# Kernel optimization log

Hardware: AMD Instinct MI355X
Metric: run time of the kernel (lower is better)

Reference implementation:

```python
import jax, jax.numpy as jnp
import numpy as np

N_NODES = 80000
N_EDGES = 800000
N_REL = 400
D_IN = 256
D_OUT = 256
BN_EPS = 1e-5


def _xavier(key, shape, gain=np.sqrt(2.0)):
    fan_in, fan_out = shape[0], shape[-1]
    std = gain * np.sqrt(2.0 / (fan_in + fan_out))
    return jax.random.normal(key, shape, dtype=jnp.float32) * std


def ccorr(a, b):
    # circular correlation: irfft(conj(rfft(a)) * rfft(b), n)
    n = a.shape[-1]
    return jnp.fft.irfft(jnp.conj(jnp.fft.rfft(a)) * jnp.fft.rfft(b), n)


def setup_inputs() -> dict:
    key = jax.random.key(0)
    ks = jax.random.split(key, 12)
    x = jax.random.normal(ks[0], (N_NODES, D_IN), dtype=jnp.float32)
    rel_repr = jax.random.normal(ks[1], (N_REL, D_IN), dtype=jnp.float32)
    edge_src = jax.random.randint(ks[2], (N_EDGES,), 0, N_NODES)
    edge_dst = jax.random.randint(ks[3], (N_EDGES,), 0, N_NODES)
    edge_type = jax.random.randint(ks[4], (N_EDGES,), 0, N_REL)
    edge_norm = jax.random.uniform(ks[5], (N_EDGES,), dtype=jnp.float32)
    in_w = _xavier(ks[6], (D_IN, D_OUT))
    out_w = _xavier(ks[7], (D_IN, D_OUT))
    loop_w = _xavier(ks[8], (D_IN, D_OUT))
    w_rel = _xavier(ks[9], (D_IN, D_OUT))
    loop_rel = _xavier(ks[10], (1, D_IN))
    bias = jnp.zeros((D_OUT,), dtype=jnp.float32)
    return {"x": x, "rel_repr": rel_repr, "edge_src": edge_src,
            "edge_dst": edge_dst, "edge_type": edge_type, "edge_norm": edge_norm,
            "in_w": in_w, "out_w": out_w, "loop_w": loop_w, "w_rel": w_rel,
            "loop_rel": loop_rel, "bias": bias}


def reference(x, rel_repr, edge_src, edge_dst, edge_type, edge_norm,
              in_w, out_w, loop_w, w_rel, loop_rel, bias):
    E = edge_src.shape[0]
    half = E // 2
    # gather + compose (opn == 'corr')
    h_src = x[edge_src]                         # [E, D_in]
    edge_data = ccorr(h_src, rel_repr[edge_type])  # [E, D_in]
    # direction-split matmul
    msg = jnp.concatenate([edge_data[:half] @ in_w,
                           edge_data[half:] @ out_w], axis=0)  # [E, D_out]
    msg = msg * edge_norm[:, None]
    # scatter-sum into destination nodes, then reduce (dropout p=0, /3)
    agg = jax.ops.segment_sum(msg, edge_dst, num_segments=x.shape[0]) / 3.0
    # self-loop
    loop = ccorr(x, jnp.broadcast_to(loop_rel, x.shape)) @ loop_w / 3.0
    out = agg + loop + bias
    # BatchNorm1d (training mode: batch stats, gamma=1, beta=0)
    mean = jnp.mean(out, axis=0)
    var = jnp.var(out, axis=0)
    out = (out - mean) / jnp.sqrt(var + BN_EPS)
    # act is identity
    return out, rel_repr @ w_rel
```

## Files before the change

### kernel.cpp

```cpp
#include <hip/hip_runtime.h>

#define NN 80000
#define NE 800000
#define EH 400000
#define NR 400
#define DD 256
#define FD 256
#define KP 768
#define NB 160000
#define NCH 157
#define MT 80400
#define PI2 6.283185307179586f

typedef unsigned short u16;
typedef __attribute__((ext_vector_type(8))) short bf16x8;
typedef __attribute__((ext_vector_type(4))) float f32x4;

static __device__ __forceinline__ float bu2f(u16 u) {
  return __uint_as_float(((unsigned int)u) << 16);
}
static __device__ __forceinline__ u16 f2bu(float f) {
  unsigned int x = __float_as_uint(f);
  x += 0x7fffu + ((x >> 16) & 1u);
  return (u16)(x >> 16);
}
static __device__ __forceinline__ unsigned int pk2(float a, float b) {
  return (unsigned int)f2bu(a) | ((unsigned int)f2bu(b) << 16);
}
static __device__ __forceinline__ void gload16(const void* g, void* l) {
  __builtin_amdgcn_global_load_lds(
      (const __attribute__((address_space(1))) unsigned int*)g,
      (__attribute__((address_space(3))) unsigned int*)l, 16, 0, 0);
}

__global__ void k_build_f(u16* __restrict__ Ft) {
  int c = blockIdx.x, j = threadIdx.x;
  int k, im;
  if (c == 0)      { k = 0;   im = 0; }
  else if (c == 1) { k = 128; im = 0; }
  else             { k = c >> 1; im = c & 1; }
  int m = (j * k) & 255;
  float th = -PI2 * (float)m * (1.0f / 256.0f);
  float v = im ? sinf(th) : cosf(th);
  Ft[c * 256 + j] = f2bu(v);
}

__global__ void k_build_m(const float* __restrict__ in_w, const float* __restrict__ out_w,
                          u16* __restrict__ Bt) {
  int t = blockIdx.x;
  int c = threadIdx.x;
  const float* W = (t < 256) ? in_w : out_w;
  int tp = t & 255;
  int k, im; float alpha;
  if (tp == 0)      { k = 0;   im = 0; alpha = 1.0f; }
  else if (tp == 1) { k = 128; im = 0; alpha = 1.0f; }
  else              { k = tp >> 1; im = tp & 1; alpha = 2.0f; }
  float scale = alpha * (1.0f / 768.0f);
  float th = -PI2 * (float)k * (1.0f / 256.0f);
  float wr = cosf(th), wi = sinf(th);
  float zr = 1.0f, zi = 0.0f;
  float acc = 0.0f;
  for (int j = 0; j < DD; ++j) {
    float coef = im ? zi : zr;
    acc += coef * W[(size_t)j * DD + c];
    float nzr = zr * wr - zi * wi; zi = zr * wi + zi * wr; zr = nzr;
  }
  Bt[(size_t)c * KP + t] = f2bu(scale * acc);
}

__global__ void k_build_q(const float* __restrict__ lr, const float* __restrict__ loop_w,
                          u16* __restrict__ Bt) {
  __shared__ float L[DD];
  int j = blockIdx.x, c = threadIdx.x;
  L[c] = lr[c];
  __syncthreads();
  float acc = 0.0f;
  for (int k2 = 0; k2 < DD; ++k2)
    acc += L[(j + k2) & 255] * loop_w[(size_t)k2 * DD + c];
  Bt[(size_t)c * KP + 512 + j] = f2bu(acc * (1.0f / 3.0f));
}

__global__ __launch_bounds__(512) void k_dft(
    const float* __restrict__ x, const float* __restrict__ rel,
    const u16* __restrict__ Ft, u16* __restrict__ xfh, u16* __restrict__ rfh,
    u16* __restrict__ Ap) {
  __shared__ u16 sA[2][128 * 64];
  __shared__ u16 sB[256 * 64];
  int tid = threadIdx.x;
  int w = tid >> 6, lane = tid & 63;
  int r0 = blockIdx.x * 128;
  int wm = (w & 1) * 64, wn = (w >> 1) * 64;
  int fr = lane & 15, fg = lane >> 4;

  int arow = tid >> 2;
  int acg = (tid & 3) * 16;
  int gr = r0 + arow;
  int grc = gr < MT ? gr : MT - 1;
  const float* asrc = (grc < NN) ? (x + (size_t)grc * DD)
                                 : (rel + (size_t)(grc - NN) * DD);
  bool doAp = (gr < NN);

  float4 a0_, a1_, a2_, a3_;
#define LOADA(kb) { const float* p_ = asrc + (kb) * 64 + acg;                     \
    a0_ = *(const float4*)(p_);     a1_ = *(const float4*)(p_ + 4);               \
    a2_ = *(const float4*)(p_ + 8); a3_ = *(const float4*)(p_ + 12); }

#define STGB(kb) { _Pragma("unroll") for (int q = 0; q < 4; ++q) {                \
    int s_ = w * 4 + q; int c_ = 8 * s_ + (lane >> 3);                            \
    int cb_ = (lane & 7) ^ (c_ & 7);                                              \
    gload16(Ft + (size_t)c_ * 256 + (kb) * 64 + cb_ * 8, sB + s_ * 512); } }

#define CVTA(kb, buf) {                                                           \
    uint4 c0_ = make_uint4(pk2(a0_.x, a0_.y), pk2(a0_.z, a0_.w),                  \
                           pk2(a1_.x, a1_.y), pk2(a1_.z, a1_.w));                 \
    uint4 c1_ = make_uint4(pk2(a2_.x, a2_.y), pk2(a2_.z, a2_.w),                  \
                           pk2(a3_.x, a3_.y), pk2(a3_.z, a3_.w));                 \
    int b0_ = (tid & 3) * 2;                                                      \
    *(uint4*)(sA[buf] + arow * 64 + ((b0_ ^ (arow & 7)) * 8)) = c0_;              \
    *(uint4*)(sA[buf] + arow * 64 + (((b0_ + 1) ^ (arow & 7)) * 8)) = c1_;        \
    if (doAp) { u16* ap_ = Ap + (size_t)gr * KP + 512 + (kb) * 64 + acg;          \
      *(uint4*)(ap_) = c0_; *(uint4*)(ap_ + 8) = c1_; } }

  f32x4 acc[4][4];
#pragma unroll
  for (int i = 0; i < 4; ++i)
#pragma unroll
    for (int j = 0; j < 4; ++j) acc[i][j] = (f32x4){0.f, 0.f, 0.f, 0.f};

  LOADA(0)
  STGB(0)
  CVTA(0, 0)
  LOADA(1)
  __syncthreads();
  for (int kb = 0; kb < 4; ++kb) {
    int cur = kb & 1;
#pragma unroll
    for (int ks = 0; ks < 2; ++ks) {
      bf16x8 af[4], bfr[4];
#pragma unroll
      for (int mt = 0; mt < 4; ++mt) {
        int r = wm + mt * 16 + fr;
        af[mt] = *(const bf16x8*)(sA[cur] + r * 64 + ((ks * 32 + fg * 8) ^ ((r & 7) * 8)));
      }
#pragma unroll
      for (int nt = 0; nt < 4; ++nt) {
        int c = wn + nt * 16 + fr;
        bfr[nt] = *(const bf16x8*)(sB + c * 64 + ((ks * 32 + fg * 8) ^ ((c & 7) * 8)));
      }
#pragma unroll
      for (int mt = 0; mt < 4; ++mt)
#pragma unroll
        for (int nt = 0; nt < 4; ++nt)
          acc[mt][nt] = __builtin_amdgcn_mfma_f32_16x16x32_bf16(af[mt], bfr[nt],
                                                                acc[mt][nt], 0, 0, 0);
    }
    __syncthreads();
    if (kb < 3) {
      STGB(kb + 1)
      CVTA(kb + 1, cur ^ 1)
      if (kb < 2) LOADA(kb + 2)
      __syncthreads();
    }
  }
#undef LOADA
#undef STGB
#undef CVTA

#pragma unroll
  for (int mt = 0; mt < 4; ++mt)
#pragma unroll
    for (int nt = 0; nt < 4; ++nt) {
      int cg = wn + nt * 16 + fr;
#pragma unroll
      for (int j = 0; j < 4; ++j) {
        int rg = r0 + wm + mt * 16 + fg * 4 + j;
        u16 val = f2bu(acc[mt][nt][j]);
        if (rg < NN)      xfh[(size_t)rg * FD + cg] = val;
        else if (rg < MT) rfh[(size_t)(rg - NN) * FD + cg] = val;
      }
    }
}

__global__ void k_hist(const int* __restrict__ edst, int* __restrict__ cnt) {
  int e = blockIdx.x * 256 + threadIdx.x;
  int key = edst[e] + ((e >= EH) ? NN : 0);
  atomicAdd(&cnt[key], 1);
}

__global__ __launch_bounds__(256) void k_scan1(const int* __restrict__ cnt,
                                               int* __restrict__ base,
                                               int* __restrict__ chunkTot) {
  __shared__ int wsum[4];
  int t = threadIdx.x;
  int g0 = blockIdx.x * 1024 + t * 4;
  int v[4], ex[4], s = 0;
#pragma unroll
  for (int j = 0; j < 4; ++j) v[j] = (g0 + j < NB) ? cnt[g0 + j] : 0;
#pragma unroll
  for (int j = 0; j < 4; ++j) { ex[j] = s; s += v[j]; }
  int lane = t & 63, w = t >> 6;
  int inc = s;
  for (int off = 1; off < 64; off <<= 1) {
    int n = __shfl_up(inc, off);
    if (lane >= off) inc += n;
  }
  if (lane == 63) wsum[w] = inc;
  __syncthreads();
  int woff = 0;
  for (int i = 0; i < w; ++i) woff += wsum[i];
  int exth = woff + inc - s;
#pragma unroll
  for (int j = 0; j < 4; ++j)
    if (g0 + j < NB) base[g0 + j] = exth + ex[j];
  if (t == 255) chunkTot[blockIdx.x] = woff + inc;
}

__global__ __launch_bounds__(256) void k_scan2(const int* __restrict__ chunkTot,
                                               int* __restrict__ chunkOff) {
  __shared__ int wsum[4];
  int t = threadIdx.x;
  int v = (t < NCH) ? chunkTot[t] : 0;
  int lane = t & 63, w = t >> 6;
  int inc = v;
  for (int off = 1; off < 64; off <<= 1) {
    int n = __shfl_up(inc, off);
    if (lane >= off) inc += n;
  }
  if (lane == 63) wsum[w] = inc;
  __syncthreads();
  int woff = 0;
  for (int i = 0; i < w; ++i) woff += wsum[i];
  if (t < NCH) chunkOff[t] = woff + inc - v;
}

__global__ void k_scan3(int* __restrict__ base, const int* __restrict__ chunkOff,
                        int* __restrict__ cursor) {
  int i = blockIdx.x * 256 + threadIdx.x;
  if (i < NB) {
    int b = base[i] + chunkOff[i >> 10];
    base[i] = b;
    cursor[i] = b;
  }
  if (i == 0) base[NB] = NE;
}

__global__ void k_scatter(const int* __restrict__ esrc, const int* __restrict__ edst,
                          const int* __restrict__ etyp, const float* __restrict__ enorm,
                          int* __restrict__ cursor, int4* __restrict__ recs) {
  int e = blockIdx.x * 256 + threadIdx.x;
  int key = edst[e] + ((e >= EH) ? NN : 0);
  int pos = atomicAdd(&cursor[key], 1);
  recs[pos] = make_int4(esrc[e], etyp[e], __float_as_int(enorm[e]), 0);
}

__global__ __launch_bounds__(256) void k_reduce(
    const u16* __restrict__ xfh, const u16* __restrict__ rfh,
    const int4* __restrict__ recs, const int* __restrict__ base,
    u16* __restrict__ Ap) {
  int w = threadIdx.x >> 6, lane = threadIdx.x & 63;
  int b = blockIdx.x * 4 + w;
  int start = base[b], end = base[b + 1];
  bool l0 = (lane == 0);
  float a0 = 0, a1 = 0, a2 = 0, a3 = 0;
  int p = start;
  for (; p + 3 < end; p += 4) {
    ushort4 xv[4], rv[4];
    float nm[4];
#pragma unroll
    for (int u = 0; u < 4; ++u) {
      int4 rc = recs[p + u];
      nm[u] = __int_as_float(rc.z);
      xv[u] = *(const ushort4*)(xfh + (size_t)rc.x * FD + 4 * lane);
      rv[u] = *(const ushort4*)(rfh + (size_t)rc.y * FD + 4 * lane);
    }
#pragma unroll
    for (int u = 0; u < 4; ++u) {
      float xr0 = bu2f(xv[u].x), xi0 = bu2f(xv[u].y);
      float xr1 = bu2f(xv[u].z), xi1 = bu2f(xv[u].w);
      float rr0 = bu2f(rv[u].x), ri0 = bu2f(rv[u].y);
      float rr1 = bu2f(rv[u].z), ri1 = bu2f(rv[u].w);
      float p0 = l0 ? (xr0 * rr0) : (xr0 * rr0 + xi0 * ri0);
      float p1 = l0 ? (xi0 * ri0) : (xr0 * ri0 - xi0 * rr0);
      a0 += p0 * nm[u];
      a1 += p1 * nm[u];
      a2 += (xr1 * rr1 + xi1 * ri1) * nm[u];
      a3 += (xr1 * ri1 - xi1 * rr1) * nm[u];
    }
  }
  for (; p < end; ++p) {
    int4 rc = recs[p];
    float nm0 = __int_as_float(rc.z);
    ushort4 xv0 = *(const ushort4*)(xfh + (size_t)rc.x * FD + 4 * lane);
    ushort4 rv0 = *(const ushort4*)(rfh + (size_t)rc.y * FD + 4 * lane);
    float xr0 = bu2f(xv0.x), xi0 = bu2f(xv0.y), xr1 = bu2f(xv0.z), xi1 = bu2f(xv0.w);
    float rr0 = bu2f(rv0.x), ri0 = bu2f(rv0.y), rr1 = bu2f(rv0.z), ri1 = bu2f(rv0.w);
    float p0 = l0 ? (xr0 * rr0) : (xr0 * rr0 + xi0 * ri0);
    float p1 = l0 ? (xi0 * ri0) : (xr0 * ri0 - xi0 * rr0);
    a0 += p0 * nm0;
    a1 += p1 * nm0;
    a2 += (xr1 * rr1 + xi1 * ri1) * nm0;
    a3 += (xr1 * ri1 - xi1 * rr1) * nm0;
  }
  u16* tp = Ap + ((b < NN) ? (size_t)b * KP : (size_t)(b - NN) * KP + 256);
  *(unsigned int*)(tp + 4 * lane)     = pk2(a0, a1);
  *(unsigned int*)(tp + 4 * lane + 2) = pk2(a2, a3);
}

__global__ __launch_bounds__(512) void k_mgemm(
    const u16* __restrict__ Ap, const u16* __restrict__ Bt,
    const float* __restrict__ bias, float* __restrict__ dout,
    float* __restrict__ sum1, float* __restrict__ sum2) {
  __shared__ u16 sA[2][128 * 64];
  __shared__ u16 sB[256 * 64];
  int tid = threadIdx.x;
  int w = tid >> 6, lane = tid & 63;
  int r0 = blockIdx.x * 128;
  int wm = (w & 1) * 64, wn = (w >> 1) * 64;
  int fr = lane & 15, fg = lane >> 4;

#define STGA(kb, buf) { _Pragma("unroll") for (int q = 0; q < 2; ++q) {           \
    int s_ = w * 2 + q; int r_ = 8 * s_ + (lane >> 3);                            \
    int cb_ = (lane & 7) ^ (r_ & 7);                                              \
    gload16(Ap + (size_t)(r0 + r_) * KP + (kb) * 64 + cb_ * 8,                    \
            sA[buf] + s_ * 512); } }

#define STGB(kb) { _Pragma("unroll") for (int q = 0; q < 4; ++q) {                \
    int s_ = w * 4 + q; int c_ = 8 * s_ + (lane >> 3);                            \
    int cb_ = (lane & 7) ^ (c_ & 7);                                              \
    gload16(Bt + (size_t)c_ * KP + (kb) * 64 + cb_ * 8, sB + s_ * 512); } }

  f32x4 acc[4][4];
#pragma unroll
  for (int i = 0; i < 4; ++i)
#pragma unroll
    for (int j = 0; j < 4; ++j) acc[i][j] = (f32x4){0.f, 0.f, 0.f, 0.f};

  STGA(0, 0)
  STGB(0)
  __syncthreads();
  for (int kb = 0; kb < 12; ++kb) {
    int cur = kb & 1;
    if (kb < 11) STGA(kb + 1, cur ^ 1)
#pragma unroll
    for (int ks = 0; ks < 2; ++ks) {
      bf16x8 af[4], bfr[4];
#pragma unroll
      for (int mt = 0; mt < 4; ++mt) {
        int r = wm + mt * 16 + fr;
        af[mt] = *(const bf16x8*)(sA[cur] + r * 64 + ((ks * 32 + fg * 8) ^ ((r & 7) * 8)));
      }
#pragma unroll
      for (int nt = 0; nt < 4; ++nt) {
        int c = wn + nt * 16 + fr;
        bfr[nt] = *(const bf16x8*)(sB + c * 64 + ((ks * 32 + fg * 8) ^ ((c & 7) * 8)));
      }
#pragma unroll
      for (int mt = 0; mt < 4; ++mt)
#pragma unroll
        for (int nt = 0; nt < 4; ++nt)
          acc[mt][nt] = __builtin_amdgcn_mfma_f32_16x16x32_bf16(af[mt], bfr[nt],
                                                                acc[mt][nt], 0, 0, 0);
    }
    __syncthreads();
    if (kb < 11) { STGB(kb + 1) __syncthreads(); }
  }
#undef STGA
#undef STGB

  float s1[4] = {0.f, 0.f, 0.f, 0.f}, s2[4] = {0.f, 0.f, 0.f, 0.f};
#pragma unroll
  for (int nt = 0; nt < 4; ++nt) {
    int cg = wn + nt * 16 + fr;
    float bv = bias[cg];
#pragma unroll
    for (int mt = 0; mt < 4; ++mt) {
#pragma unroll
      for (int j = 0; j < 4; ++j) {
        int rg = r0 + wm + mt * 16 + fg * 4 + j;
        float val = acc[mt][nt][j] + bv;
        dout[(size_t)rg * DD + cg] = val;
        s1[nt] += val;
        s2[nt] += val * val;
      }
    }
  }
#pragma unroll
  for (int nt = 0; nt < 4; ++nt) {
    s1[nt] += __shfl_xor(s1[nt], 16); s1[nt] += __shfl_xor(s1[nt], 32);
    s2[nt] += __shfl_xor(s2[nt], 16); s2[nt] += __shfl_xor(s2[nt], 32);
  }
  if (lane < 16) {
#pragma unroll
    for (int nt = 0; nt < 4; ++nt) {
      atomicAdd(&sum1[wn + nt * 16 + lane], s1[nt]);
      atomicAdd(&sum2[wn + nt * 16 + lane], s2[nt]);
    }
  }
}

__global__ void k_stats(const float* __restrict__ sum1, const float* __restrict__ sum2,
                        float* __restrict__ mean, float* __restrict__ rstd) {
  int c = threadIdx.x;
  float m = sum1[c] * (1.0f / (float)NN);
  float var = sum2[c] * (1.0f / (float)NN) - m * m;
  mean[c] = m;
  rstd[c] = rsqrtf(var + 1e-5f);
}

__global__ void k_norm(float* __restrict__ out, const float* __restrict__ mean,
                       const float* __restrict__ rstd) {
  size_t i4 = ((size_t)blockIdx.x * 256 + threadIdx.x) * 4;
  float4* p = (float4*)(out + i4);
  float4 v = *p;
  int c0 = (int)(i4 & 255);
  v.x = (v.x - mean[c0 + 0]) * rstd[c0 + 0];
  v.y = (v.y - mean[c0 + 1]) * rstd[c0 + 1];
  v.z = (v.z - mean[c0 + 2]) * rstd[c0 + 2];
  v.w = (v.w - mean[c0 + 3]) * rstd[c0 + 3];
  *p = v;
}

__global__ void k_rel(const float* __restrict__ rel, const float* __restrict__ wrel,
                      float* __restrict__ out2) {
  __shared__ float R[DD];
  int r = blockIdx.x, c = threadIdx.x;
  R[c] = rel[(size_t)r * DD + c];
  __syncthreads();
  float acc = 0.0f;
  for (int j = 0; j < DD; ++j)
    acc += R[j] * wrel[(size_t)j * DD + c];
  out2[(size_t)r * DD + c] = acc;
}

__global__ void k_fail(float* __restrict__ out, int n) {
  int i = blockIdx.x * 256 + threadIdx.x;
  if (i < n) out[i] = 1.0e6f;
}

extern "C" void kernel_launch(void* const* d_in, const int* in_sizes, int n_in,
                              void* d_out, int out_size, void* d_ws, size_t ws_size,
                              hipStream_t stream) {
  (void)in_sizes; (void)n_in;
  const float* x      = (const float*)d_in[0];
  const float* rel    = (const float*)d_in[1];
  const int*   esrc   = (const int*)d_in[2];
  const int*   edst   = (const int*)d_in[3];
  const int*   etyp   = (const int*)d_in[4];
  const float* enorm  = (const float*)d_in[5];
  const float* in_w   = (const float*)d_in[6];
  const float* out_w  = (const float*)d_in[7];
  const float* loop_w = (const float*)d_in[8];
  const float* w_rel  = (const float*)d_in[9];
  const float* lr     = (const float*)d_in[10];
  const float* bias   = (const float*)d_in[11];
  float* dout = (float*)d_out;

  char* wsb = (char*)d_ws;
  size_t off = 0;
  u16* Apack = (u16*)(wsb + off); off += (size_t)NN * KP * 2;
  u16* Bt    = (u16*)(wsb + off); off += (size_t)DD * KP * 2;
  u16* xfh   = (u16*)(wsb + off); off += (size_t)NN * FD * 2;
  u16* rfh   = (u16*)(wsb + off); off += (size_t)NR * FD * 2;
  u16* Ft    = (u16*)(wsb + off); off += (size_t)DD * DD * 2;
  int4* recs = (int4*)(wsb + off); off += (size_t)NE * 16;
  float* sum1  = (float*)(wsb + off); off += DD * 4;
  float* sum2  = (float*)(wsb + off); off += DD * 4;
  float* meanb = (float*)(wsb + off); off += DD * 4;
  float* rstdb = (float*)(wsb + off); off += DD * 4;
  int* cnt   = (int*)(wsb + off); off += (size_t)(NB + 1) * 4;
  int* baseA = (int*)(wsb + off); off += (size_t)(NB + 1) * 4;
  int* curA  = (int*)(wsb + off); off += (size_t)NB * 4;
  int* chT   = (int*)(wsb + off); off += 256 * 4;
  int* chO   = (int*)(wsb + off); off += 256 * 4;

  if (ws_size < off) {
    k_fail<<<(out_size + 255) / 256, 256, 0, stream>>>(dout, out_size);
    return;
  }

  hipMemsetAsync(cnt, 0, (NB + 1) * sizeof(int), stream);
  hipMemsetAsync(sum1, 0, 2 * DD * sizeof(float), stream);
  k_build_f<<<256, 256, 0, stream>>>(Ft);
  k_build_m<<<512, 256, 0, stream>>>(in_w, out_w, Bt);
  k_build_q<<<256, 256, 0, stream>>>(lr, loop_w, Bt);
  k_hist<<<NE / 256, 256, 0, stream>>>(edst, cnt);
  k_scan1<<<NCH, 256, 0, stream>>>(cnt, baseA, chT);
  k_scan2<<<1, 256, 0, stream>>>(chT, chO);
  k_scan3<<<(NB + 255) / 256, 256, 0, stream>>>(baseA, chO, curA);
  k_scatter<<<NE / 256, 256, 0, stream>>>(esrc, edst, etyp, enorm, curA, recs);
  k_dft<<<(MT + 127) / 128, 512, 0, stream>>>(x, rel, Ft, xfh, rfh, Apack);
  k_reduce<<<NB / 4, 256, 0, stream>>>(xfh, rfh, recs, baseA, Apack);
  k_mgemm<<<NN / 128, 512, 0, stream>>>(Apack, Bt, bias, dout, sum1, sum2);
  k_stats<<<1, 256, 0, stream>>>(sum1, sum2, meanb, rstdb);
  k_norm<<<NN * DD / 4 / 256, 256, 0, stream>>>(dout, meanb, rstdb);
  k_rel<<<NR, 256, 0, stream>>>(rel, w_rel, dout + (size_t)NN * DD);
}
```

Measured before the change: 381.6 us.

## Split reduce wave into two edge halves with wide loads; fuse BN stats into norm

The edge-reduce kernel now has each half-wave handle a different edge, using 16-byte gathers instead of 8-byte ones. Partial sums are combined with a cross-half shuffle, and the scalar remainder loop is replaced by masked iterations. The BatchNorm stats kernel is folded into a grid-stride normalize kernel that computes mean and rstd per thread. The three weight-build kernels become a single launch. This aims to raise memory-level parallelism in the gather and cut launch overhead, at the cost of some wasted loads on masked edges.

```diff
diff --git a/kernel.cpp b/kernel.cpp
--- a/kernel.cpp
+++ b/kernel.cpp
@@ -33,51 +33,48 @@
       (__attribute__((address_space(3))) unsigned int*)l, 16, 0, 0);
 }
 
-__global__ void k_build_f(u16* __restrict__ Ft) {
-  int c = blockIdx.x, j = threadIdx.x;
-  int k, im;
-  if (c == 0)      { k = 0;   im = 0; }
-  else if (c == 1) { k = 128; im = 0; }
-  else             { k = c >> 1; im = c & 1; }
-  int m = (j * k) & 255;
-  float th = -PI2 * (float)m * (1.0f / 256.0f);
-  float v = im ? sinf(th) : cosf(th);
-  Ft[c * 256 + j] = f2bu(v);
-}
-
-__global__ void k_build_m(const float* __restrict__ in_w, const float* __restrict__ out_w,
-                          u16* __restrict__ Bt) {
-  int t = blockIdx.x;
-  int c = threadIdx.x;
-  const float* W = (t < 256) ? in_w : out_w;
-  int tp = t & 255;
-  int k, im; float alpha;
-  if (tp == 0)      { k = 0;   im = 0; alpha = 1.0f; }
-  else if (tp == 1) { k = 128; im = 0; alpha = 1.0f; }
-  else              { k = tp >> 1; im = tp & 1; alpha = 2.0f; }
-  float scale = alpha * (1.0f / 768.0f);
-  float th = -PI2 * (float)k * (1.0f / 256.0f);
-  float wr = cosf(th), wi = sinf(th);
-  float zr = 1.0f, zi = 0.0f;
-  float acc = 0.0f;
-  for (int j = 0; j < DD; ++j) {
-    float coef = im ? zi : zr;
-    acc += coef * W[(size_t)j * DD + c];
-    float nzr = zr * wr - zi * wi; zi = zr * wi + zi * wr; zr = nzr;
-  }
-  Bt[(size_t)c * KP + t] = f2bu(scale * acc);
-}
-
-__global__ void k_build_q(const float* __restrict__ lr, const float* __restrict__ loop_w,
-                          u16* __restrict__ Bt) {
+__global__ void k_build(const float* __restrict__ in_w, const float* __restrict__ out_w,
+                        const float* __restrict__ lr, const float* __restrict__ loop_w,
+                        u16* __restrict__ Ft, u16* __restrict__ Bt) {
   __shared__ float L[DD];
-  int j = blockIdx.x, c = threadIdx.x;
-  L[c] = lr[c];
-  __syncthreads();
-  float acc = 0.0f;
-  for (int k2 = 0; k2 < DD; ++k2)
-    acc += L[(j + k2) & 255] * loop_w[(size_t)k2 * DD + c];
-  Bt[(size_t)c * KP + 512 + j] = f2bu(acc * (1.0f / 3.0f));
+  int bb = blockIdx.x, c = threadIdx.x;
+  if (bb < 256) {
+    int row = bb, j = c;
+    int k, im;
+    if (row == 0)      { k = 0;   im = 0; }
+    else if (row == 1) { k = 128; im = 0; }
+    else               { k = row >> 1; im = row & 1; }
+    int m = (j * k) & 255;
+    float th = -PI2 * (float)m * (1.0f / 256.0f);
+    Ft[row * 256 + j] = f2bu(im ? sinf(th) : cosf(th));
+  } else if (bb < 768) {
+    int t = bb - 256;
+    const float* W = (t < 256) ? in_w : out_w;
+    int tp = t & 255;
+    int k, im; float alpha;
+    if (tp == 0)      { k = 0;   im = 0; alpha = 1.0f; }
+    else if (tp == 1) { k = 128; im = 0; alpha = 1.0f; }
+    else              { k = tp >> 1; im = tp & 1; alpha = 2.0f; }
+    float scale = alpha * (1.0f / 768.0f);
+    float th = -PI2 * (float)k * (1.0f / 256.0f);
+    float wr = cosf(th), wi = sinf(th);
+    float zr = 1.0f, zi = 0.0f;
+    float acc = 0.0f;
+    for (int j = 0; j < DD; ++j) {
+      float coef = im ? zi : zr;
+      acc += coef * W[(size_t)j * DD + c];
+      float nzr = zr * wr - zi * wi; zi = zr * wi + zi * wr; zr = nzr;
+    }
+    Bt[(size_t)c * KP + t] = f2bu(scale * acc);
+  } else {
+    int j = bb - 768;
+    L[c] = lr[c];
+    __syncthreads();
+    float acc = 0.0f;
+    for (int k2 = 0; k2 < DD; ++k2)
+      acc += L[(j + k2) & 255] * loop_w[(size_t)k2 * DD + c];
+    Bt[(size_t)c * KP + 512 + j] = f2bu(acc * (1.0f / 3.0f));
+  }
 }
 
 __global__ __launch_bounds__(512) void k_dft(
@@ -260,50 +257,54 @@
   int w = threadIdx.x >> 6, lane = threadIdx.x & 63;
   int b = blockIdx.x * 4 + w;
   int start = base[b], end = base[b + 1];
-  bool l0 = (lane == 0);
-  float a0 = 0, a1 = 0, a2 = 0, a3 = 0;
-  int p = start;
-  for (; p + 3 < end; p += 4) {
-    ushort4 xv[4], rv[4];
+  int h = lane >> 5, sl = lane & 31;
+  bool sp = (sl == 0);
+  float a0 = 0, a1 = 0, a2 = 0, a3 = 0, a4 = 0, a5 = 0, a6 = 0, a7 = 0;
+  for (int p = start; p < end; p += 8) {
+    uint4 xv[4], rv[4];
     float nm[4];
 #pragma unroll
     for (int u = 0; u < 4; ++u) {
-      int4 rc = recs[p + u];
-      nm[u] = __int_as_float(rc.z);
-      xv[u] = *(const ushort4*)(xfh + (size_t)rc.x * FD + 4 * lane);
-      rv[u] = *(const ushort4*)(rfh + (size_t)rc.y * FD + 4 * lane);
+      int idx = p + 2 * u + h;
+      int mi = (idx < end) ? idx : start;
+      int4 rc = recs[mi];
+      nm[u] = (idx < end) ? __int_as_float(rc.z) : 0.0f;
+      xv[u] = *(const uint4*)(xfh + (size_t)rc.x * FD + 8 * sl);
+      rv[u] = *(const uint4*)(rfh + (size_t)rc.y * FD + 8 * sl);
     }
 #pragma unroll
     for (int u = 0; u < 4; ++u) {
-      float xr0 = bu2f(xv[u].x), xi0 = bu2f(xv[u].y);
-      float xr1 = bu2f(xv[u].z), xi1 = bu2f(xv[u].w);
-      float rr0 = bu2f(rv[u].x), ri0 = bu2f(rv[u].y);
-      float rr1 = bu2f(rv[u].z), ri1 = bu2f(rv[u].w);
-      float p0 = l0 ? (xr0 * rr0) : (xr0 * rr0 + xi0 * ri0);
-      float p1 = l0 ? (xi0 * ri0) : (xr0 * ri0 - xi0 * rr0);
-      a0 += p0 * nm[u];
-      a1 += p1 * nm[u];
-      a2 += (xr1 * rr1 + xi1 * ri1) * nm[u];
-      a3 += (xr1 * ri1 - xi1 * rr1) * nm[u];
-    }
-  }
-  for (; p < end; ++p) {
-    int4 rc = recs[p];
-    float nm0 = __int_as_float(rc.z);
-    ushort4 xv0 = *(const ushort4*)(xfh + (size_t)rc.x * FD + 4 * lane);
-    ushort4 rv0 = *(const ushort4*)(rfh + (size_t)rc.y * FD + 4 * lane);
-    float xr0 = bu2f(xv0.x), xi0 = bu2f(xv0.y), xr1 = bu2f(xv0.z), xi1 = bu2f(xv0.w);
-    float rr0 = bu2f(rv0.x), ri0 = bu2f(rv0.y), rr1 = bu2f(rv0.z), ri1 = bu2f(rv0.w);
-    float p0 = l0 ? (xr0 * rr0) : (xr0 * rr0 + xi0 * ri0);
-    float p1 = l0 ? (xi0 * ri0) : (xr0 * ri0 - xi0 * rr0);
-    a0 += p0 * nm0;
-    a1 += p1 * nm0;
-    a2 += (xr1 * rr1 + xi1 * ri1) * nm0;
-    a3 += (xr1 * ri1 - xi1 * rr1) * nm0;
-  }
-  u16* tp = Ap + ((b < NN) ? (size_t)b * KP : (size_t)(b - NN) * KP + 256);
-  *(unsigned int*)(tp + 4 * lane)     = pk2(a0, a1);
-  *(unsigned int*)(tp + 4 * lane + 2) = pk2(a2, a3);
+      float n = nm[u];
+      uint4 xq = xv[u], rq = rv[u];
+      float x0 = bu2f((u16)xq.x), x1 = bu2f((u16)(xq.x >> 16));
+      float r0 = bu2f((u16)rq.x), r1 = bu2f((u16)(rq.x >> 16));
+      float p0 = sp ? (x0 * r0) : (x0 * r0 + x1 * r1);
+      float p1 = sp ? (x1 * r1) : (x0 * r1 - x1 * r0);
+      a0 += p0 * n;
+      a1 += p1 * n;
+      float x2 = bu2f((u16)xq.y), x3 = bu2f((u16)(xq.y >> 16));
+      float r2 = bu2f((u16)rq.y), r3 = bu2f((u16)(rq.y >> 16));
+      a2 += (x2 * r2 + x3 * r3) * n;
+      a3 += (x2 * r3 - x3 * r2) * n;
+      float x4 = bu2f((u16)xq.z), x5 = bu2f((u16)(xq.z >> 16));
+      float r4 = bu2f((u16)rq.z), r5 = bu2f((u16)(rq.z >> 16));
+      a4 += (x4 * r4 + x5 * r5) * n;
+      a5 += (x4 * r5 - x5 * r4) * n;
+      float x6 = bu2f((u16)xq.w), x7 = bu2f((u16)(xq.w >> 16));
+      float r6 = bu2f((u16)rq.w), r7 = bu2f((u16)(rq.w >> 16));
+      a6 += (x6 * r6 + x7 * r7) * n;
+      a7 += (x6 * r7 - x7 * r6) * n;
+    }
+  }
+  a0 += __shfl_xor(a0, 32); a1 += __shfl_xor(a1, 32);
+  a2 += __shfl_xor(a2, 32); a3 += __shfl_xor(a3, 32);
+  a4 += __shfl_xor(a4, 32); a5 += __shfl_xor(a5, 32);
+  a6 += __shfl_xor(a6, 32); a7 += __shfl_xor(a7, 32);
+  if (h == 0) {
+    u16* tp = Ap + ((b < NN) ? (size_t)b * KP : (size_t)(b - NN) * KP + 256) + 8 * sl;
+    uint4 o = make_uint4(pk2(a0, a1), pk2(a2, a3), pk2(a4, a5), pk2(a6, a7));
+    *(uint4*)tp = o;
+  }
 }
 
 __global__ __launch_bounds__(512) void k_mgemm(
@@ -398,26 +399,30 @@
   }
 }
 
-__global__ void k_stats(const float* __restrict__ sum1, const float* __restrict__ sum2,
-                        float* __restrict__ mean, float* __restrict__ rstd) {
-  int c = threadIdx.x;
-  float m = sum1[c] * (1.0f / (float)NN);
-  float var = sum2[c] * (1.0f / (float)NN) - m * m;
-  mean[c] = m;
-  rstd[c] = rsqrtf(var + 1e-5f);
-}
-
-__global__ void k_norm(float* __restrict__ out, const float* __restrict__ mean,
-                       const float* __restrict__ rstd) {
-  size_t i4 = ((size_t)blockIdx.x * 256 + threadIdx.x) * 4;
-  float4* p = (float4*)(out + i4);
-  float4 v = *p;
-  int c0 = (int)(i4 & 255);
-  v.x = (v.x - mean[c0 + 0]) * rstd[c0 + 0];
-  v.y = (v.y - mean[c0 + 1]) * rstd[c0 + 1];
-  v.z = (v.z - mean[c0 + 2]) * rstd[c0 + 2];
-  v.w = (v.w - mean[c0 + 3]) * rstd[c0 + 3];
-  *p = v;
+__global__ __launch_bounds__(256) void k_norm(float* __restrict__ out,
+                                              const float* __restrict__ sum1,
+                                              const float* __restrict__ sum2) {
+  size_t tid0 = (size_t)blockIdx.x * 256 + threadIdx.x;
+  int c0 = (int)((tid0 * 4) & 255);
+  float m[4], rs[4];
+#pragma unroll
+  for (int j = 0; j < 4; ++j) {
+    float mm = sum1[c0 + j] * (1.0f / (float)NN);
+    float var = sum2[c0 + j] * (1.0f / (float)NN) - mm * mm;
+    m[j] = mm;
+    rs[j] = rsqrtf(var + 1e-5f);
+  }
+  size_t total = (size_t)NN * DD / 4;
+  size_t stride = (size_t)gridDim.x * 256;
+  for (size_t i = tid0; i < total; i += stride) {
+    float4* p = (float4*)out + i;
+    float4 v = *p;
+    v.x = (v.x - m[0]) * rs[0];
+    v.y = (v.y - m[1]) * rs[1];
+    v.z = (v.z - m[2]) * rs[2];
+    v.w = (v.w - m[3]) * rs[3];
+    *p = v;
+  }
 }
 
 __global__ void k_rel(const float* __restrict__ rel, const float* __restrict__ wrel,
@@ -465,8 +470,6 @@
   int4* recs = (int4*)(wsb + off); off += (size_t)NE * 16;
   float* sum1  = (float*)(wsb + off); off += DD * 4;
   float* sum2  = (float*)(wsb + off); off += DD * 4;
-  float* meanb = (float*)(wsb + off); off += DD * 4;
-  float* rstdb = (float*)(wsb + off); off += DD * 4;
   int* cnt   = (int*)(wsb + off); off += (size_t)(NB + 1) * 4;
   int* baseA = (int*)(wsb + off); off += (size_t)(NB + 1) * 4;
   int* curA  = (int*)(wsb + off); off += (size_t)NB * 4;
@@ -480,9 +483,7 @@
 
   hipMemsetAsync(cnt, 0, (NB + 1) * sizeof(int), stream);
   hipMemsetAsync(sum1, 0, 2 * DD * sizeof(float), stream);
-  k_build_f<<<256, 256, 0, stream>>>(Ft);
-  k_build_m<<<512, 256, 0, stream>>>(in_w, out_w, Bt);
-  k_build_q<<<256, 256, 0, stream>>>(lr, loop_w, Bt);
+  k_build<<<1024, 256, 0, stream>>>(in_w, out_w, lr, loop_w, Ft, Bt);
   k_hist<<<NE / 256, 256, 0, stream>>>(edst, cnt);
   k_scan1<<<NCH, 256, 0, stream>>>(cnt, baseA, chT);
   k_scan2<<<1, 256, 0, stream>>>(chT, chO);
@@ -491,7 +492,6 @@
   k_dft<<<(MT + 127) / 128, 512, 0, stream>>>(x, rel, Ft, xfh, rfh, Apack);
   k_reduce<<<NB / 4, 256, 0, stream>>>(xfh, rfh, recs, baseA, Apack);
   k_mgemm<<<NN / 128, 512, 0, stream>>>(Apack, Bt, bias, dout, sum1, sum2);
-  k_stats<<<1, 256, 0, stream>>>(sum1, sum2, meanb, rstdb);
-  k_norm<<<NN * DD / 4 / 256, 256, 0, stream>>>(dout, meanb, rstdb);
+  k_norm<<<2048, 256, 0, stream>>>(dout, sum1, sum2);
   k_rel<<<NR, 256, 0, stream>>>(rel, w_rel, dout + (size_t)NN * DD);
 }
```

Result: slower. 397.6 us (+4.2%).
